# Optimization experiments

Hardware: AMD Instinct MI355X
Metric: run time of the kernel (lower is better)

Reference implementation:

```python
import jax, jax.numpy as jnp
import numpy as np


def setup_inputs() -> dict:
    key = jax.random.key(0)
    k1, k2, k3, k4 = jax.random.split(key, 4)
    n, c, p1, p2, r = 8, 3, 512, 512, 8
    X = jax.random.uniform(k1, (n, c, p1, p2), dtype=jnp.float32)
    S = jax.random.uniform(k2, (c, r), dtype=jnp.float32)
    S = S / (jnp.linalg.norm(S, axis=0, keepdims=True))  # unit-norm columns like S_init
    gamma = jax.random.uniform(k3, (1,), dtype=jnp.float32) * 1e-05
    lam = jax.random.uniform(k4, (1,), dtype=jnp.float32) * 1e-05
    return {"X": X, "S": S, "gamma": gamma, "lam": lam, "n_iter": 2}


def reference(X, S, gamma, lam, n_iter):
    n, c, p1, p2 = X.shape
    p = p1 * p2
    r = S.shape[1]
    Xf = X.reshape(n, c, p)
    gamma = jnp.abs(gamma)
    lam = jnp.abs(lam)
    Dt = jnp.zeros((n, r, p), dtype=X.dtype)
    x0 = jnp.mean(Xf, axis=2, keepdims=True)
    for _ in range(n_iter):
        # ---- D update (proximal gradient) ----
        SDt = jnp.einsum('cr,nrp->ncp', S, Dt)  # S @ Dt
        x0 = jnp.mean(Xf + SDt, axis=2, keepdims=True)  # [n,c,1]
        tau_D = 1.0 / jnp.sum(S * S)  # 1/||S||_F^2
        Dt = Dt - tau_D * jnp.einsum('cr,ncp->nrp', S, SDt + Xf - x0)
        S_nrm = jnp.linalg.norm(S, axis=0).reshape(1, r, 1)  # [1,r,1]
        Dt = jax.nn.relu(Dt - lam * gamma * tau_D * S_nrm)
        Dt_L2 = jnp.linalg.norm(Dt, axis=2, keepdims=True)  # [n,r,1]
        scl = jax.nn.relu(Dt_L2 - lam * tau_D * S_nrm)
        scl = scl / Dt_L2 + 1e-10  # faithful to source (eps added after divide)
        Dt = Dt * scl
        # ---- S update (proximal gradient) ----
        SDt = jnp.einsum('cr,nrp->ncp', S, Dt)
        x0 = jnp.mean(Xf + SDt, axis=2, keepdims=True)
        Dt_sum = jnp.sum(Dt, axis=2, keepdims=True)  # [n,r,1]
        tau_S = 1.0 / jnp.mean(jnp.sum(Dt * Dt, axis=(1, 2)))
        grad = jnp.mean(
            jnp.einsum('ncp,nqp->ncq', SDt + Xf, Dt)
            - x0 @ jnp.transpose(Dt_sum, (0, 2, 1)),
            axis=0)  # [c,r]
        S_grad = S - tau_S * grad
        Dt_nrm = jnp.mean(
            gamma * jnp.sum(jnp.abs(Dt), axis=2, keepdims=True)
            + jnp.linalg.norm(Dt, axis=2, keepdims=True), axis=0)  # [r,1]
        Sg_nrm = jnp.linalg.norm(S_grad, axis=0, keepdims=True)  # [1,r]
        scl_S = jax.nn.relu(Sg_nrm - lam * tau_S * Dt_nrm.T)
        scl_S = scl_S / (Sg_nrm + 1e-10)
        S = S_grad * scl_S
        # ---- unit-norm rescale (unit_norm_S=True) ----
        S_nrm2 = jnp.linalg.norm(S, axis=0, keepdims=True)  # [1,r]
        S = S / (S_nrm2 + 1e-10)
        Dt = Dt * (S_nrm2.reshape(1, r, 1) + 1e-10)
    return x0, S, Dt.reshape(n, r, p1, p2)
```

## Files before the change

kernel.cpp:

```cpp
#include <hip/hip_runtime.h>

constexpr int N = 8, C = 3, R = 8;
constexpr int P = 512 * 512;
constexpr int BLK = 256;
constexpr int NB = 128;
constexpr int PPB = P / NB;
constexpr int PITER = PPB / (BLK * 4);
constexpr int NBF = 256;
constexpr int PPBF = P / NBF;
constexpr int NK = 68;

typedef float f32x4 __attribute__((ext_vector_type(4)));

constexpr int W_XSUM  = 0;
constexpr int W_S1    = 32;
constexpr int W_F1    = 64;
constexpr int W_THR2  = 128;
constexpr int W_TAU2  = 136;
constexpr int W_SNRM2 = 144;
constexpr int W_X02   = 160;
constexpr int W_F2    = 192;
constexpr int W_RED   = 256;
constexpr int W_PART  = 1024;

#define XR8(M) M(0) M(1) M(2) M(3) M(4) M(5) M(6) M(7)
#define XTRI(M) \
  M(0,0) \
  M(1,0) M(1,1) \
  M(2,0) M(2,1) M(2,2) \
  M(3,0) M(3,1) M(3,2) M(3,3) \
  M(4,0) M(4,1) M(4,2) M(4,3) M(4,4) \
  M(5,0) M(5,1) M(5,2) M(5,3) M(5,4) M(5,5) \
  M(6,0) M(6,1) M(6,2) M(6,3) M(6,4) M(6,5) M(6,6) \
  M(7,0) M(7,1) M(7,2) M(7,3) M(7,4) M(7,5) M(7,6) M(7,7)
#define XCR(M) \
  M(0,0) M(0,1) M(0,2) M(0,3) M(0,4) M(0,5) M(0,6) M(0,7) \
  M(1,0) M(1,1) M(1,2) M(1,3) M(1,4) M(1,5) M(1,6) M(1,7) \
  M(2,0) M(2,1) M(2,2) M(2,3) M(2,4) M(2,5) M(2,6) M(2,7)

__device__ __forceinline__ float sld(float x) {
    return __uint_as_float(__builtin_amdgcn_readfirstlane(__float_as_uint(x)));
}
__device__ __forceinline__ float waveSum(float v) {
    #pragma unroll
    for (int o = 32; o > 0; o >>= 1) v += __shfl_down(v, o);
    return v;
}

__device__ __forceinline__ float rowSum16(float v) {
    int x;
    x = __builtin_amdgcn_update_dpp(0, __float_as_int(v), 0xB1, 0xF, 0xF, true);
    v += __int_as_float(x);
    x = __builtin_amdgcn_update_dpp(0, __float_as_int(v), 0x4E, 0xF, 0xF, true);
    v += __int_as_float(x);
    x = __builtin_amdgcn_update_dpp(0, __float_as_int(v), 0x124, 0xF, 0xF, true);
    v += __int_as_float(x);
    x = __builtin_amdgcn_update_dpp(0, __float_as_int(v), 0x128, 0xF, 0xF, true);
    v += __int_as_float(x);
    return v;
}

__global__ __launch_bounds__(BLK)
void k_xmean(const float* __restrict__ X, float* __restrict__ ws) {
    int nc = blockIdx.y;
    int t = threadIdx.x;
    size_t base = (size_t)nc * P + (size_t)blockIdx.x * 4096;
    float s = 0.f;
    #pragma unroll
    for (int i = 0; i < 4; ++i) {
        float4 q = *(const float4*)(X + base + (size_t)(i * BLK + t) * 4);
        s += (q.x + q.y) + (q.z + q.w);
    }
    __shared__ float red[16];
    s = rowSum16(s);
    if ((t & 15) == 0) red[t >> 4] = s;
    __syncthreads();
    if (t == 0) {
        float a = 0.f;
        #pragma unroll
        for (int g = 0; g < 16; ++g) a += red[g];
        atomicAdd(ws + W_XSUM + nc, a);
    }
}

__global__ __launch_bounds__(64)
void k_red(const float* __restrict__ part, float* __restrict__ ws) {
    int g = blockIdx.x, t = threadIdx.x;
    const float* p = part + (size_t)g * NB;
    float s = p[t] + p[t + 64];
    s = waveSum(s);
    if (t == 0) ws[W_RED + g] = s;
}

#define C_P1(r) const float p_##r = fmaxf(fmaf(-tau1c, fmaf(S0_0##r, tt0, fmaf(S0_1##r, tt1, S0_2##r * tt2)), -th1_##r), 0.f);
#define C_AL(r) const float a_##r = p_##r;
#define C_D2(r) const float d_##r = f1_##r * p_##r;
#define C_W(c)  const float w##c = fmaf(S1_##c##0, d_0, fmaf(S1_##c##1, d_1, fmaf(S1_##c##2, d_2, fmaf(S1_##c##3, d_3, fmaf(S1_##c##4, d_4, fmaf(S1_##c##5, d_5, fmaf(S1_##c##6, d_6, fmaf(S1_##c##7, d_7, tt##c + dx0_##c))))))));
#define C_A2(r) const float a_##r = fmaxf(fmaf(-tau2c, fmaf(S1_0##r, w0, fmaf(S1_1##r, w1, S1_2##r * w2)), d_##r - th2_##r), 0.f);
#define AC_T(q,r) tq_##q##_##r = fmaf(a_##r, a_##q, tq_##q##_##r);
#define AC_SM(r)  sm_##r += a_##r;
#define AC_V(c,q) vv_##c##_##q = fmaf(tt##c, a_##q, vv_##c##_##q);
#define GXc(q) (q).x
#define GYc(q) (q).y
#define GZc(q) (q).z
#define GWc(q) (q).w

template <int MODE>
__global__ __launch_bounds__(BLK)
void k_dstats(const float* __restrict__ X, const float* __restrict__ Sin,
              const float* __restrict__ gp, const float* __restrict__ lp,
              const float* __restrict__ ws, float* __restrict__ part) {
    const int n = blockIdx.y, t = threadIdx.x;
    const float lamv = fabsf(*lp), gamv = fabsf(*gp);
    const float invP = 1.0f / (float)P;

    float ssq0 = 0.f;
    #pragma unroll
    for (int i = 0; i < 24; ++i) { float v = Sin[i]; ssq0 = fmaf(v, v, ssq0); }
    const float tau1c = sld(1.0f / ssq0);
#define LD_TH1(r) const float th1_##r = sld(lamv * gamv * tau1c * sqrtf(fmaf(Sin[r], Sin[r], fmaf(Sin[8 + r], Sin[8 + r], Sin[16 + r] * Sin[16 + r]))));
    XR8(LD_TH1)
    const float x01_0 = sld(ws[W_XSUM + n * 3 + 0] * invP);
    const float x01_1 = sld(ws[W_XSUM + n * 3 + 1] * invP);
    const float x01_2 = sld(ws[W_XSUM + n * 3 + 2] * invP);
#define LD_S0(c,q) const float S0_##c##q = sld(Sin[(c) * 8 + (q)]);
    XCR(LD_S0)
#define LD_S1(c,q) const float S1_##c##q = (MODE >= 1) ? sld(ws[W_S1 + (c) * 8 + (q)]) : 0.f;
    XCR(LD_S1)
#define LD_F1(r)  const float f1_##r = (MODE >= 1) ? sld(ws[W_F1 + n * 8 + (r)]) : 0.f;
#define LD_TH2(r) const float th2_##r = (MODE >= 1) ? sld(ws[W_THR2 + (r)]) : 0.f;
    XR8(LD_F1) XR8(LD_TH2)
    const float tau2c = (MODE >= 1) ? sld(ws[W_TAU2]) : 0.f;
    const float dx0_0 = (MODE >= 1) ? sld(x01_0 - ws[W_X02 + n * 3 + 0]) : 0.f;
    const float dx0_1 = (MODE >= 1) ? sld(x01_1 - ws[W_X02 + n * 3 + 1]) : 0.f;
    const float dx0_2 = (MODE >= 1) ? sld(x01_2 - ws[W_X02 + n * 3 + 2]) : 0.f;

    const float* Xn = X + (size_t)n * C * P;
    const int rsel = t & 15, rowid = t >> 4;

#define SITE_T(GET) { \
    const float tt0 = GET(xv0) - x01_0; \
    const float tt1 = GET(xv1) - x01_1; \
    const float tt2 = GET(xv2) - x01_2; \
    XR8(C_P1) \
    if constexpr (MODE == 0) { XR8(C_AL) XTRI(AC_T) } \
    else { XR8(C_D2) C_W(0) C_W(1) C_W(2) XR8(C_A2) XTRI(AC_T) } }

#define SITE_SV(GET) { \
    const float tt0 = GET(xv0) - x01_0; \
    const float tt1 = GET(xv1) - x01_1; \
    const float tt2 = GET(xv2) - x01_2; \
    XR8(C_P1) \
    if constexpr (MODE == 0) { XR8(C_AL) XR8(AC_SM) XCR(AC_V) } \
    else { XR8(C_D2) C_W(0) C_W(1) C_W(2) XR8(C_A2) XR8(AC_SM) XCR(AC_V) } }

    if (blockIdx.z == 0) {
#define D_T(q,r) float tq_##q##_##r = 0.f;
        XTRI(D_T)
        #pragma unroll
        for (int it = 0; it < PITER; ++it) {
            size_t pbase = (size_t)blockIdx.x * PPB + (size_t)(it * BLK + t) * 4;
            float4 xv0 = *(const float4*)(Xn + 0 * (size_t)P + pbase);
            float4 xv1 = *(const float4*)(Xn + 1 * (size_t)P + pbase);
            float4 xv2 = *(const float4*)(Xn + 2 * (size_t)P + pbase);
            SITE_T(GXc) SITE_T(GYc) SITE_T(GZc) SITE_T(GWc)
        }
        __shared__ float redT[36][16];
#define RDT(q,r) { constexpr int kk = (q) * ((q) + 1) / 2 + (r); \
                   float v = rowSum16(tq_##q##_##r); \
                   if (rsel == (kk & 15)) redT[kk][rowid] = v; }
        XTRI(RDT)
        __syncthreads();
        if (t < 36) {
            const float* row = redT[t];
            float s = 0.f;
            #pragma unroll
            for (int g = 0; g < 16; ++g) s += row[g];
            part[((size_t)(8 + t) * N + n) * NB + blockIdx.x] = s;
        }
    } else {
#define D_SM(r)  float sm_##r = 0.f;
#define D_V(c,q) float vv_##c##_##q = 0.f;
        XR8(D_SM) XCR(D_V)
        #pragma unroll
        for (int it = 0; it < PITER; ++it) {
            size_t pbase = (size_t)blockIdx.x * PPB + (size_t)(it * BLK + t) * 4;
            float4 xv0 = *(const float4*)(Xn + 0 * (size_t)P + pbase);
            float4 xv1 = *(const float4*)(Xn + 1 * (size_t)P + pbase);
            float4 xv2 = *(const float4*)(Xn + 2 * (size_t)P + pbase);
            SITE_SV(GXc) SITE_SV(GYc) SITE_SV(GZc) SITE_SV(GWc)
        }
        __shared__ float redS[32][16];
#define RDS(r)   { constexpr int kk = (r); \
                   float v = rowSum16(sm_##r); \
                   if (rsel == (kk & 15)) redS[kk][rowid] = v; }
#define RDV(c,q) { constexpr int kk = 8 + (c) * 8 + (q); \
                   float v = rowSum16(vv_##c##_##q); \
                   if (rsel == (kk & 15)) redS[kk][rowid] = v; }
        XR8(RDS) XCR(RDV)
        __syncthreads();
        if (t < 32) {
            const float* row = redS[t];
            float s = 0.f;
            #pragma unroll
            for (int g = 0; g < 16; ++g) s += row[g];
            int krow = (t < 8) ? t : 44 + (t - 8);
            part[((size_t)krow * N + n) * NB + blockIdx.x] = s;
        }
    }
}

template <int IT>
__global__ __launch_bounds__(64)
void k_t23(const float* __restrict__ Sin, const float* __restrict__ gp,
           const float* __restrict__ lp, float* __restrict__ ws,
           float* __restrict__ x0_out, float* __restrict__ S_out) {
    const int t = threadIdx.x;
    const float invP = 1.0f / (float)P;
    const float lam_ = fabsf(*lp), gam_ = fabsf(*gp);
    __shared__ float sum_[N][R], T_[N][R][R], U_[N][C][R];
    __shared__ float scl_[N][R], L2_[N][R], x0s_[N][C], dtn_[R];
    __shared__ float Scur_[24], oS[24], oF[64], grad_[24], snrmI[8], pn_[8];
    __shared__ float tauS_, tauD_;
    for (int i = t; i < NK * N; i += 64) {
        int k = i / N, nn = i % N;
        float v = ws[W_RED + i];
        if (k < 8) sum_[nn][k] = v;
        else if (k < 44) {
            int m = k - 8; int q = 0;
            while ((q + 1) * (q + 2) / 2 <= m) ++q;
            int r = m - q * (q + 1) / 2;
            T_[nn][r][q] = v; T_[nn][q][r] = v;
        } else { int m = k - 44; U_[nn][m >> 3][m & 7] = v; }
    }
    if (t < 24) Scur_[t] = IT ? ws[W_S1 + t] : Sin[t];
    if (t == 0) {
        if (IT) tauD_ = ws[W_TAU2];
        else { float s = 0.f; for (int i = 0; i < 24; ++i) s += Sin[i] * Sin[i]; tauD_ = 1.0f / s; }
    }
    if (t < 8) {
        if (IT) snrmI[t] = ws[W_SNRM2 + t];
        else snrmI[t] = sqrtf(Sin[t] * Sin[t] + Sin[8 + t] * Sin[8 + t] + Sin[16 + t] * Sin[16 + t]);
    }
    __syncthreads();
    for (int i = t; i < N * C * R; i += 64) {
        int nn = i / 24, m = i % 24, c = m >> 3, q = m & 7;
        U_[nn][c][q] += ws[W_XSUM + nn * 3 + c] * invP * sum_[nn][q];
    }
    if (t < 64) {
        int nn = t >> 3, r = t & 7;
        float l2 = sqrtf(T_[nn][r][r]);
        float scl = fmaxf(l2 - lam_ * tauD_ * snrmI[r], 0.f) / l2 + 1e-10f;
        scl_[nn][r] = scl; L2_[nn][r] = l2;
    }
    __syncthreads();
    if (t == 0) {
        float tot = 0.f;
        for (int nn = 0; nn < N; ++nn)
            for (int r = 0; r < R; ++r)
                tot += scl_[nn][r] * scl_[nn][r] * T_[nn][r][r];
        tauS_ = (float)N / tot;
    }
    if (t < 24) {
        int nn = t / 3, c = t % 3;
        float acc = ws[W_XSUM + t] * invP;
        #pragma unroll
        for (int r = 0; r < R; ++r)
            acc += Scur_[c * R + r] * scl_[nn][r] * sum_[nn][r] * invP;
        x0s_[nn][c] = acc;
        if (IT == 1) x0_out[t] = acc;
    }
    if (t >= 32 && t < 40) {
        int r = t - 32;
        float a = 0.f;
        #pragma unroll
        for (int nn = 0; nn < N; ++nn)
            a += scl_[nn][r] * (gam_ * sum_[nn][r] + L2_[nn][r]);
        dtn_[r] = a * (1.0f / N);
    }
    __syncthreads();
    if (t < 24) {
        int c = t / 8, q = t % 8;
        float a = 0.f;
        #pragma unroll
        for (int nn = 0; nn < N; ++nn) {
            float m = U_[nn][c][q];
            #pragma unroll
            for (int r = 0; r < R; ++r)
                m += Scur_[c * R + r] * scl_[nn][r] * T_[nn][r][q];
            a += scl_[nn][q] * (m - x0s_[nn][c] * sum_[nn][q]);
        }
        grad_[t] = a * (1.0f / N);
    }
    __syncthreads();
    if (t == 0) {
        float Sg[24], Sn[24];
        #pragma unroll
        for (int i = 0; i < 24; ++i) Sg[i] = Scur_[i] - tauS_ * grad_[i];
        #pragma unroll
        for (int q = 0; q < 8; ++q) {
            float s2 = 0.f;
            #pragma unroll
            for (int c = 0; c < 3; ++c) s2 += Sg[c * 8 + q] * Sg[c * 8 + q];
            float sgn = sqrtf(s2);
            float s = fmaxf(sgn - lam_ * tauS_ * dtn_[q], 0.f) / (sgn + 1e-10f);
            #pragma unroll
            for (int c = 0; c < 3; ++c) Sn[c * 8 + q] = Sg[c * 8 + q] * s;
        }
        #pragma unroll
        for (int q = 0; q < 8; ++q) {
            float s2 = 0.f;
            #pragma unroll
            for (int c = 0; c < 3; ++c) s2 += Sn[c * 8 + q] * Sn[c * 8 + q];
            float n2 = sqrtf(s2);
            pn_[q] = n2;
            #pragma unroll
            for (int c = 0; c < 3; ++c) oS[c * 8 + q] = Sn[c * 8 + q] / (n2 + 1e-10f);
        }
        if (IT == 0) {
            float ssq = 0.f;
            #pragma unroll
            for (int i = 0; i < 24; ++i) ssq += oS[i] * oS[i];
            float tau2 = 1.0f / ssq;
            ws[W_TAU2] = tau2;
            #pragma unroll
            for (int r = 0; r < 8; ++r) {
                float cn = sqrtf(oS[r] * oS[r] + oS[8 + r] * oS[8 + r] + oS[16 + r] * oS[16 + r]);
                ws[W_SNRM2 + r] = cn;
                ws[W_THR2 + r] = lam_ * gam_ * tau2 * cn;
            }
        }
    }
    __syncthreads();
    if (t < 64) oF[t] = scl_[t >> 3][t & 7] * (pn_[t & 7] + 1e-10f);
    __syncthreads();
    if (IT == 0) {
        if (t < 24) {
            int nn = t / 3, c = t % 3;
            float acc = ws[W_XSUM + t] * invP;
            #pragma unroll
            for (int r = 0; r < R; ++r)
                acc += oS[c * R + r] * oF[nn * R + r] * sum_[nn][r] * invP;
            ws[W_X02 + t] = acc;
            ws[W_S1 + t] = oS[t];
        }
        if (t < 64) ws[W_F1 + t] = oF[t];
    } else {
        if (t < 24) S_out[t] = oS[t];
        if (t < 64) ws[W_F2 + t] = oF[t];
    }
}

__global__ __launch_bounds__(BLK)
void k_dfinal(const float* __restrict__ X, const float* __restrict__ Sin,
              const float* __restrict__ gp, const float* __restrict__ lp,
              const float* __restrict__ ws, float* __restrict__ Dt_out) {
    const int n = blockIdx.y, t = threadIdx.x;
    const float lamv = fabsf(*lp), gamv = fabsf(*gp);
    const float invP = 1.0f / (float)P;
    float ssq0 = 0.f;
    #pragma unroll
    for (int i = 0; i < 24; ++i) { float v = Sin[i]; ssq0 = fmaf(v, v, ssq0); }
    const float tau1c = sld(1.0f / ssq0);
    XR8(LD_TH1)
    const float x01_0 = sld(ws[W_XSUM + n * 3 + 0] * invP);
    const float x01_1 = sld(ws[W_XSUM + n * 3 + 1] * invP);
    const float x01_2 = sld(ws[W_XSUM + n * 3 + 2] * invP);
    XCR(LD_S0)
#define LD2_S1(c,q) const float S1_##c##q = sld(ws[W_S1 + (c) * 8 + (q)]);
#define LD2_F1(r)  const float f1_##r = sld(ws[W_F1 + n * 8 + (r)]);
#define LD2_TH2(r) const float th2_##r = sld(ws[W_THR2 + (r)]);
#define LD2_F2(r)  const float f2_##r = sld(ws[W_F2 + n * 8 + (r)]);
    XCR(LD2_S1) XR8(LD2_F1) XR8(LD2_TH2) XR8(LD2_F2)
    const float tau2c = sld(ws[W_TAU2]);
    const float dx0_0 = sld(x01_0 - ws[W_X02 + n * 3 + 0]);
    const float dx0_1 = sld(x01_1 - ws[W_X02 + n * 3 + 1]);
    const float dx0_2 = sld(x01_2 - ws[W_X02 + n * 3 + 2]);

    const float* Xn = X + (size_t)n * C * P;
    float* Dn = Dt_out + (size_t)n * R * P;

#define PXc(r) ov_##r.x = f2_##r * a_##r;
#define PYc(r) ov_##r.y = f2_##r * a_##r;
#define PZc(r) ov_##r.z = f2_##r * a_##r;
#define PWc(r) ov_##r.w = f2_##r * a_##r;
#define SITE_F(GET, PUTM) { \
    const float tt0 = GET(xv0) - x01_0; \
    const float tt1 = GET(xv1) - x01_1; \
    const float tt2 = GET(xv2) - x01_2; \
    XR8(C_P1) XR8(C_D2) C_W(0) C_W(1) C_W(2) XR8(C_A2) XR8(PUTM) }
#define D_OV(r) float4 ov_##r;
#define ST_O(r) *(float4*)(Dn + (size_t)(r) * P + pbase) = ov_##r;
    {
        size_t pbase = (size_t)blockIdx.x * PPBF + (size_t)t * 4;
        float4 xv0 = *(const float4*)(Xn + 0 * (size_t)P + pbase);
        float4 xv1 = *(const float4*)(Xn + 1 * (size_t)P + pbase);
        float4 xv2 = *(const float4*)(Xn + 2 * (size_t)P + pbase);
        XR8(D_OV)
        SITE_F(GXc, PXc) SITE_F(GYc, PYc) SITE_F(GZc, PZc) SITE_F(GWc, PWc)
        XR8(ST_O)
    }
}

extern "C" void kernel_launch(void* const* d_in, const int* in_sizes, int n_in,
                              void* d_out, int out_size, void* d_ws, size_t ws_size,
                              hipStream_t stream) {
    const float* X   = (const float*)d_in[0];
    const float* Sin = (const float*)d_in[1];
    const float* gam = (const float*)d_in[2];
    const float* lam = (const float*)d_in[3];
    float* out    = (float*)d_out;
    float* x0_out = out;
    float* S_out  = out + 24;
    float* Dt_out = out + 48;
    float* ws     = (float*)d_ws;
    float* part   = ws + W_PART;

    hipMemsetAsync(ws, 0, 24 * sizeof(float), stream);
    k_xmean<<<dim3(64, N * C), BLK, 0, stream>>>(X, ws);

    k_dstats<0><<<dim3(NB, N, 2), BLK, 0, stream>>>(X, Sin, gam, lam, ws, part);
    k_red<<<NK * N, 64, 0, stream>>>(part, ws);
    k_t23<0><<<1, 64, 0, stream>>>(Sin, gam, lam, ws, x0_out, S_out);

    k_dstats<1><<<dim3(NB, N, 2), BLK, 0, stream>>>(X, Sin, gam, lam, ws, part);
    k_red<<<NK * N, 64, 0, stream>>>(part, ws);
    k_t23<1><<<1, 64, 0, stream>>>(Sin, gam, lam, ws, x0_out, S_out);

    k_dfinal<<<dim3(NBF, N), BLK, 0, stream>>>(X, Sin, gam, lam, ws, Dt_out);
}
```

Baseline: 102.4 us.

## Replace partial-sum reduction kernels with atomics and recompute tiny solver per block

Per-block partial statistics are now accumulated directly with global atomicAdd instead of written to a partial buffer and reduced by a separate kernel. The single-block S-update kernels are removed, and their small math is recomputed redundantly at the start of every block of the next stats kernel and of the final kernel. This cuts the launch count from nine to five and removes two serialized tiny kernels. In exchange, every block repeats the tiny solver, including __syncthreads steps, before its main loop. Atomic accumulation also makes the floating-point summation order nondeterministic.

```diff
diff --git a/kernel.cpp b/kernel.cpp
--- a/kernel.cpp
+++ b/kernel.cpp
@@ -12,16 +12,10 @@
 
 typedef float f32x4 __attribute__((ext_vector_type(4)));
 
-constexpr int W_XSUM  = 0;
-constexpr int W_S1    = 32;
-constexpr int W_F1    = 64;
-constexpr int W_THR2  = 128;
-constexpr int W_TAU2  = 136;
-constexpr int W_SNRM2 = 144;
-constexpr int W_X02   = 160;
-constexpr int W_F2    = 192;
-constexpr int W_RED   = 256;
-constexpr int W_PART  = 1024;
+constexpr int W_XSUM = 0;
+constexpr int W_ACC1 = 32;
+constexpr int W_ACC2 = 608;
+constexpr int W_ZEND = 1152;
 
 #define XR8(M) M(0) M(1) M(2) M(3) M(4) M(5) M(6) M(7)
 #define XTRI(M) \
@@ -41,12 +35,6 @@
 __device__ __forceinline__ float sld(float x) {
     return __uint_as_float(__builtin_amdgcn_readfirstlane(__float_as_uint(x)));
 }
-__device__ __forceinline__ float waveSum(float v) {
-    #pragma unroll
-    for (int o = 32; o > 0; o >>= 1) v += __shfl_down(v, o);
-    return v;
-}
-
 __device__ __forceinline__ float rowSum16(float v) {
     int x;
     x = __builtin_amdgcn_update_dpp(0, __float_as_int(v), 0xB1, 0xF, 0xF, true);
@@ -83,13 +71,140 @@
     }
 }
 
-__global__ __launch_bounds__(64)
-void k_red(const float* __restrict__ part, float* __restrict__ ws) {
-    int g = blockIdx.x, t = threadIdx.x;
-    const float* p = part + (size_t)g * NB;
-    float s = p[t] + p[t + 64];
-    s = waveSum(s);
-    if (t == 0) ws[W_RED + g] = s;
+template <int IT>
+__device__ void t23_math(const float* __restrict__ accG, const float* __restrict__ SinG,
+                         const float* __restrict__ iS, const float* __restrict__ iTau,
+                         const float* __restrict__ iCN, const float* __restrict__ ws,
+                         float lam_, float gam_,
+                         float* oS, float* oF, float* oTH2, float* oTAU2,
+                         float* oCN, float* oX02, float* ox0s) {
+    const int t = threadIdx.x;
+    const float invP = 1.0f / (float)P;
+    __shared__ float sum_[N][R], T_[N][R][R], U_[N][C][R];
+    __shared__ float scl_[N][R], L2_[N][R], x0s_[N][C], dtn_[R];
+    __shared__ float Scur_[24], grad_[24], snrmI[8], pn_[8];
+    __shared__ float tauS_, tauD_;
+    for (int i = t; i < NK * N; i += BLK) {
+        int k = i / N, nn = i % N;
+        float v = accG[i];
+        if (k < 8) sum_[nn][k] = v;
+        else if (k < 44) {
+            int m = k - 8; int q = 0;
+            while ((q + 1) * (q + 2) / 2 <= m) ++q;
+            int r = m - q * (q + 1) / 2;
+            T_[nn][r][q] = v; T_[nn][q][r] = v;
+        } else { int m = k - 44; U_[nn][m >> 3][m & 7] = v; }
+    }
+    if (t < 24) Scur_[t] = IT ? iS[t] : SinG[t];
+    if (t == 0) {
+        if (IT) tauD_ = iTau[0];
+        else { float s = 0.f; for (int i = 0; i < 24; ++i) s += SinG[i] * SinG[i]; tauD_ = 1.0f / s; }
+    }
+    if (t < 8) {
+        if (IT) snrmI[t] = iCN[t];
+        else snrmI[t] = sqrtf(SinG[t] * SinG[t] + SinG[8 + t] * SinG[8 + t] + SinG[16 + t] * SinG[16 + t]);
+    }
+    __syncthreads();
+    for (int i = t; i < N * C * R; i += BLK) {
+        int nn = i / 24, m = i % 24, c = m >> 3, q = m & 7;
+        U_[nn][c][q] += ws[W_XSUM + nn * 3 + c] * invP * sum_[nn][q];
+    }
+    if (t < 64) {
+        int nn = t >> 3, r = t & 7;
+        float l2 = sqrtf(T_[nn][r][r]);
+        float scl = fmaxf(l2 - lam_ * tauD_ * snrmI[r], 0.f) / l2 + 1e-10f;
+        scl_[nn][r] = scl; L2_[nn][r] = l2;
+    }
+    __syncthreads();
+    if (t == 0) {
+        float tot = 0.f;
+        for (int nn = 0; nn < N; ++nn)
+            for (int r = 0; r < R; ++r)
+                tot += scl_[nn][r] * scl_[nn][r] * T_[nn][r][r];
+        tauS_ = (float)N / tot;
+    }
+    if (t < 24) {
+        int nn = t / 3, c = t % 3;
+        float acc = ws[W_XSUM + t] * invP;
+        #pragma unroll
+        for (int r = 0; r < R; ++r)
+            acc += Scur_[c * R + r] * scl_[nn][r] * sum_[nn][r] * invP;
+        x0s_[nn][c] = acc;
+        if (IT == 1) ox0s[t] = acc;
+    }
+    if (t >= 32 && t < 40) {
+        int r = t - 32;
+        float a = 0.f;
+        #pragma unroll
+        for (int nn = 0; nn < N; ++nn)
+            a += scl_[nn][r] * (gam_ * sum_[nn][r] + L2_[nn][r]);
+        dtn_[r] = a * (1.0f / N);
+    }
+    __syncthreads();
+    if (t < 24) {
+        int c = t / 8, q = t % 8;
+        float a = 0.f;
+        #pragma unroll
+        for (int nn = 0; nn < N; ++nn) {
+            float m = U_[nn][c][q];
+            #pragma unroll
+            for (int r = 0; r < R; ++r)
+                m += Scur_[c * R + r] * scl_[nn][r] * T_[nn][r][q];
+            a += scl_[nn][q] * (m - x0s_[nn][c] * sum_[nn][q]);
+        }
+        grad_[t] = a * (1.0f / N);
+    }
+    __syncthreads();
+    if (t == 0) {
+        float Sg[24], Sn[24];
+        #pragma unroll
+        for (int i = 0; i < 24; ++i) Sg[i] = Scur_[i] - tauS_ * grad_[i];
+        #pragma unroll
+        for (int q = 0; q < 8; ++q) {
+            float s2 = 0.f;
+            #pragma unroll
+            for (int c = 0; c < 3; ++c) s2 += Sg[c * 8 + q] * Sg[c * 8 + q];
+            float sgn = sqrtf(s2);
+            float s = fmaxf(sgn - lam_ * tauS_ * dtn_[q], 0.f) / (sgn + 1e-10f);
+            #pragma unroll
+            for (int c = 0; c < 3; ++c) Sn[c * 8 + q] = Sg[c * 8 + q] * s;
+        }
+        #pragma unroll
+        for (int q = 0; q < 8; ++q) {
+            float s2 = 0.f;
+            #pragma unroll
+            for (int c = 0; c < 3; ++c) s2 += Sn[c * 8 + q] * Sn[c * 8 + q];
+            float n2 = sqrtf(s2);
+            pn_[q] = n2;
+            #pragma unroll
+            for (int c = 0; c < 3; ++c) oS[c * 8 + q] = Sn[c * 8 + q] / (n2 + 1e-10f);
+        }
+        if (IT == 0) {
+            float ssq = 0.f;
+            #pragma unroll
+            for (int i = 0; i < 24; ++i) ssq += oS[i] * oS[i];
+            float tau2 = 1.0f / ssq;
+            oTAU2[0] = tau2;
+            #pragma unroll
+            for (int r = 0; r < 8; ++r) {
+                float cn = sqrtf(oS[r] * oS[r] + oS[8 + r] * oS[8 + r] + oS[16 + r] * oS[16 + r]);
+                oCN[r] = cn;
+                oTH2[r] = lam_ * gam_ * tau2 * cn;
+            }
+        }
+    }
+    __syncthreads();
+    if (t < 64) oF[t] = scl_[t >> 3][t & 7] * (pn_[t & 7] + 1e-10f);
+    __syncthreads();
+    if (IT == 0 && t < 24) {
+        int nn = t / 3, c = t % 3;
+        float acc = ws[W_XSUM + t] * invP;
+        #pragma unroll
+        for (int r = 0; r < R; ++r)
+            acc += oS[c * R + r] * oF[nn * R + r] * sum_[nn][r] * invP;
+        oX02[t] = acc;
+    }
+    __syncthreads();
 }
 
 #define C_P1(r) const float p_##r = fmaxf(fmaf(-tau1c, fmaf(S0_0##r, tt0, fmaf(S0_1##r, tt1, S0_2##r * tt2)), -th1_##r), 0.f);
@@ -109,10 +224,16 @@
 __global__ __launch_bounds__(BLK)
 void k_dstats(const float* __restrict__ X, const float* __restrict__ Sin,
               const float* __restrict__ gp, const float* __restrict__ lp,
-              const float* __restrict__ ws, float* __restrict__ part) {
+              float* __restrict__ ws) {
     const int n = blockIdx.y, t = threadIdx.x;
     const float lamv = fabsf(*lp), gamv = fabsf(*gp);
     const float invP = 1.0f / (float)P;
+
+    __shared__ float oS[24], oF[64], oTH2[8], oTAU2[1], oCN[8], oX02[24];
+    if constexpr (MODE == 1) {
+        t23_math<0>(ws + W_ACC1, Sin, nullptr, nullptr, nullptr, ws, lamv, gamv,
+                    oS, oF, oTH2, oTAU2, oCN, oX02, nullptr);
+    }
 
     float ssq0 = 0.f;
     #pragma unroll
@@ -125,18 +246,19 @@
     const float x01_2 = sld(ws[W_XSUM + n * 3 + 2] * invP);
 #define LD_S0(c,q) const float S0_##c##q = sld(Sin[(c) * 8 + (q)]);
     XCR(LD_S0)
-#define LD_S1(c,q) const float S1_##c##q = (MODE >= 1) ? sld(ws[W_S1 + (c) * 8 + (q)]) : 0.f;
+#define LD_S1(c,q) const float S1_##c##q = (MODE >= 1) ? sld(oS[(c) * 8 + (q)]) : 0.f;
     XCR(LD_S1)
-#define LD_F1(r)  const float f1_##r = (MODE >= 1) ? sld(ws[W_F1 + n * 8 + (r)]) : 0.f;
-#define LD_TH2(r) const float th2_##r = (MODE >= 1) ? sld(ws[W_THR2 + (r)]) : 0.f;
+#define LD_F1(r)  const float f1_##r = (MODE >= 1) ? sld(oF[n * 8 + (r)]) : 0.f;
+#define LD_TH2(r) const float th2_##r = (MODE >= 1) ? sld(oTH2[(r)]) : 0.f;
     XR8(LD_F1) XR8(LD_TH2)
-    const float tau2c = (MODE >= 1) ? sld(ws[W_TAU2]) : 0.f;
-    const float dx0_0 = (MODE >= 1) ? sld(x01_0 - ws[W_X02 + n * 3 + 0]) : 0.f;
-    const float dx0_1 = (MODE >= 1) ? sld(x01_1 - ws[W_X02 + n * 3 + 1]) : 0.f;
-    const float dx0_2 = (MODE >= 1) ? sld(x01_2 - ws[W_X02 + n * 3 + 2]) : 0.f;
+    const float tau2c = (MODE >= 1) ? sld(oTAU2[0]) : 0.f;
+    const float dx0_0 = (MODE >= 1) ? sld(x01_0 - oX02[n * 3 + 0]) : 0.f;
+    const float dx0_1 = (MODE >= 1) ? sld(x01_1 - oX02[n * 3 + 1]) : 0.f;
+    const float dx0_2 = (MODE >= 1) ? sld(x01_2 - oX02[n * 3 + 2]) : 0.f;
 
     const float* Xn = X + (size_t)n * C * P;
     const int rsel = t & 15, rowid = t >> 4;
+    float* accOut = ws + (MODE == 0 ? W_ACC1 : W_ACC2);
 
 #define SITE_T(GET) { \
     const float tt0 = GET(xv0) - x01_0; \
@@ -176,7 +298,7 @@
             float s = 0.f;
             #pragma unroll
             for (int g = 0; g < 16; ++g) s += row[g];
-            part[((size_t)(8 + t) * N + n) * NB + blockIdx.x] = s;
+            atomicAdd(accOut + (8 + t) * N + n, s);
         }
     } else {
 #define D_SM(r)  float sm_##r = 0.f;
@@ -205,159 +327,28 @@
             #pragma unroll
             for (int g = 0; g < 16; ++g) s += row[g];
             int krow = (t < 8) ? t : 44 + (t - 8);
-            part[((size_t)krow * N + n) * NB + blockIdx.x] = s;
-        }
-    }
-}
-
-template <int IT>
-__global__ __launch_bounds__(64)
-void k_t23(const float* __restrict__ Sin, const float* __restrict__ gp,
-           const float* __restrict__ lp, float* __restrict__ ws,
-           float* __restrict__ x0_out, float* __restrict__ S_out) {
-    const int t = threadIdx.x;
-    const float invP = 1.0f / (float)P;
-    const float lam_ = fabsf(*lp), gam_ = fabsf(*gp);
-    __shared__ float sum_[N][R], T_[N][R][R], U_[N][C][R];
-    __shared__ float scl_[N][R], L2_[N][R], x0s_[N][C], dtn_[R];
-    __shared__ float Scur_[24], oS[24], oF[64], grad_[24], snrmI[8], pn_[8];
-    __shared__ float tauS_, tauD_;
-    for (int i = t; i < NK * N; i += 64) {
-        int k = i / N, nn = i % N;
-        float v = ws[W_RED + i];
-        if (k < 8) sum_[nn][k] = v;
-        else if (k < 44) {
-            int m = k - 8; int q = 0;
-            while ((q + 1) * (q + 2) / 2 <= m) ++q;
-            int r = m - q * (q + 1) / 2;
-            T_[nn][r][q] = v; T_[nn][q][r] = v;
-        } else { int m = k - 44; U_[nn][m >> 3][m & 7] = v; }
-    }
-    if (t < 24) Scur_[t] = IT ? ws[W_S1 + t] : Sin[t];
-    if (t == 0) {
-        if (IT) tauD_ = ws[W_TAU2];
-        else { float s = 0.f; for (int i = 0; i < 24; ++i) s += Sin[i] * Sin[i]; tauD_ = 1.0f / s; }
-    }
-    if (t < 8) {
-        if (IT) snrmI[t] = ws[W_SNRM2 + t];
-        else snrmI[t] = sqrtf(Sin[t] * Sin[t] + Sin[8 + t] * Sin[8 + t] + Sin[16 + t] * Sin[16 + t]);
-    }
-    __syncthreads();
-    for (int i = t; i < N * C * R; i += 64) {
-        int nn = i / 24, m = i % 24, c = m >> 3, q = m & 7;
-        U_[nn][c][q] += ws[W_XSUM + nn * 3 + c] * invP * sum_[nn][q];
-    }
-    if (t < 64) {
-        int nn = t >> 3, r = t & 7;
-        float l2 = sqrtf(T_[nn][r][r]);
-        float scl = fmaxf(l2 - lam_ * tauD_ * snrmI[r], 0.f) / l2 + 1e-10f;
-        scl_[nn][r] = scl; L2_[nn][r] = l2;
-    }
-    __syncthreads();
-    if (t == 0) {
-        float tot = 0.f;
-        for (int nn = 0; nn < N; ++nn)
-            for (int r = 0; r < R; ++r)
-                tot += scl_[nn][r] * scl_[nn][r] * T_[nn][r][r];
-        tauS_ = (float)N / tot;
-    }
-    if (t < 24) {
-        int nn = t / 3, c = t % 3;
-        float acc = ws[W_XSUM + t] * invP;
-        #pragma unroll
-        for (int r = 0; r < R; ++r)
-            acc += Scur_[c * R + r] * scl_[nn][r] * sum_[nn][r] * invP;
-        x0s_[nn][c] = acc;
-        if (IT == 1) x0_out[t] = acc;
-    }
-    if (t >= 32 && t < 40) {
-        int r = t - 32;
-        float a = 0.f;
-        #pragma unroll
-        for (int nn = 0; nn < N; ++nn)
-            a += scl_[nn][r] * (gam_ * sum_[nn][r] + L2_[nn][r]);
-        dtn_[r] = a * (1.0f / N);
-    }
-    __syncthreads();
-    if (t < 24) {
-        int c = t / 8, q = t % 8;
-        float a = 0.f;
-        #pragma unroll
-        for (int nn = 0; nn < N; ++nn) {
-            float m = U_[nn][c][q];
-            #pragma unroll
-            for (int r = 0; r < R; ++r)
-                m += Scur_[c * R + r] * scl_[nn][r] * T_[nn][r][q];
-            a += scl_[nn][q] * (m - x0s_[nn][c] * sum_[nn][q]);
-        }
-        grad_[t] = a * (1.0f / N);
-    }
-    __syncthreads();
-    if (t == 0) {
-        float Sg[24], Sn[24];
-        #pragma unroll
-        for (int i = 0; i < 24; ++i) Sg[i] = Scur_[i] - tauS_ * grad_[i];
-        #pragma unroll
-        for (int q = 0; q < 8; ++q) {
-            float s2 = 0.f;
-            #pragma unroll
-            for (int c = 0; c < 3; ++c) s2 += Sg[c * 8 + q] * Sg[c * 8 + q];
-            float sgn = sqrtf(s2);
-            float s = fmaxf(sgn - lam_ * tauS_ * dtn_[q], 0.f) / (sgn + 1e-10f);
-            #pragma unroll
-            for (int c = 0; c < 3; ++c) Sn[c * 8 + q] = Sg[c * 8 + q] * s;
-        }
-        #pragma unroll
-        for (int q = 0; q < 8; ++q) {
-            float s2 = 0.f;
-            #pragma unroll
-            for (int c = 0; c < 3; ++c) s2 += Sn[c * 8 + q] * Sn[c * 8 + q];
-            float n2 = sqrtf(s2);
-            pn_[q] = n2;
-            #pragma unroll
-            for (int c = 0; c < 3; ++c) oS[c * 8 + q] = Sn[c * 8 + q] / (n2 + 1e-10f);
-        }
-        if (IT == 0) {
-            float ssq = 0.f;
-            #pragma unroll
-            for (int i = 0; i < 24; ++i) ssq += oS[i] * oS[i];
-            float tau2 = 1.0f / ssq;
-            ws[W_TAU2] = tau2;
-            #pragma unroll
-            for (int r = 0; r < 8; ++r) {
-                float cn = sqrtf(oS[r] * oS[r] + oS[8 + r] * oS[8 + r] + oS[16 + r] * oS[16 + r]);
-                ws[W_SNRM2 + r] = cn;
-                ws[W_THR2 + r] = lam_ * gam_ * tau2 * cn;
-            }
-        }
-    }
-    __syncthreads();
-    if (t < 64) oF[t] = scl_[t >> 3][t & 7] * (pn_[t & 7] + 1e-10f);
-    __syncthreads();
-    if (IT == 0) {
-        if (t < 24) {
-            int nn = t / 3, c = t % 3;
-            float acc = ws[W_XSUM + t] * invP;
-            #pragma unroll
-            for (int r = 0; r < R; ++r)
-                acc += oS[c * R + r] * oF[nn * R + r] * sum_[nn][r] * invP;
-            ws[W_X02 + t] = acc;
-            ws[W_S1 + t] = oS[t];
-        }
-        if (t < 64) ws[W_F1 + t] = oF[t];
-    } else {
-        if (t < 24) S_out[t] = oS[t];
-        if (t < 64) ws[W_F2 + t] = oF[t];
+            atomicAdd(accOut + krow * N + n, s);
+        }
     }
 }
 
 __global__ __launch_bounds__(BLK)
 void k_dfinal(const float* __restrict__ X, const float* __restrict__ Sin,
               const float* __restrict__ gp, const float* __restrict__ lp,
-              const float* __restrict__ ws, float* __restrict__ Dt_out) {
+              float* __restrict__ ws, float* __restrict__ Dt_out,
+              float* __restrict__ x0_out, float* __restrict__ S_out) {
     const int n = blockIdx.y, t = threadIdx.x;
     const float lamv = fabsf(*lp), gamv = fabsf(*gp);
     const float invP = 1.0f / (float)P;
+
+    __shared__ float oS[24], oF[64], oTH2[8], oTAU2[1], oCN[8], oX02[24];
+    __shared__ float oS2[24], oF2[64], oTH2b[8], oTAU2b[1], oCNb[8], oX02b[24], ox0s[24];
+    t23_math<0>(ws + W_ACC1, Sin, nullptr, nullptr, nullptr, ws, lamv, gamv,
+                oS, oF, oTH2, oTAU2, oCN, oX02, nullptr);
+    t23_math<1>(ws + W_ACC2, nullptr, oS, oTAU2, oCN, ws, lamv, gamv,
+                oS2, oF2, oTH2b, oTAU2b, oCNb, oX02b, ox0s);
+    if (blockIdx.x == 0 && n == 0 && t < 24) { x0_out[t] = ox0s[t]; S_out[t] = oS2[t]; }
+
     float ssq0 = 0.f;
     #pragma unroll
     for (int i = 0; i < 24; ++i) { float v = Sin[i]; ssq0 = fmaf(v, v, ssq0); }
@@ -367,15 +358,15 @@
     const float x01_1 = sld(ws[W_XSUM + n * 3 + 1] * invP);
     const float x01_2 = sld(ws[W_XSUM + n * 3 + 2] * invP);
     XCR(LD_S0)
-#define LD2_S1(c,q) const float S1_##c##q = sld(ws[W_S1 + (c) * 8 + (q)]);
-#define LD2_F1(r)  const float f1_##r = sld(ws[W_F1 + n * 8 + (r)]);
-#define LD2_TH2(r) const float th2_##r = sld(ws[W_THR2 + (r)]);
-#define LD2_F2(r)  const float f2_##r = sld(ws[W_F2 + n * 8 + (r)]);
-    XCR(LD2_S1) XR8(LD2_F1) XR8(LD2_TH2) XR8(LD2_F2)
-    const float tau2c = sld(ws[W_TAU2]);
-    const float dx0_0 = sld(x01_0 - ws[W_X02 + n * 3 + 0]);
-    const float dx0_1 = sld(x01_1 - ws[W_X02 + n * 3 + 1]);
-    const float dx0_2 = sld(x01_2 - ws[W_X02 + n * 3 + 2]);
+#define LDF_S1(c,q) const float S1_##c##q = sld(oS[(c) * 8 + (q)]);
+#define LDF_F1(r)  const float f1_##r = sld(oF[n * 8 + (r)]);
+#define LDF_TH2(r) const float th2_##r = sld(oTH2[(r)]);
+#define LDF_F2(r)  const float f2_##r = sld(oF2[n * 8 + (r)]);
+    XCR(LDF_S1) XR8(LDF_F1) XR8(LDF_TH2) XR8(LDF_F2)
+    const float tau2c = sld(oTAU2[0]);
+    const float dx0_0 = sld(x01_0 - oX02[n * 3 + 0]);
+    const float dx0_1 = sld(x01_1 - oX02[n * 3 + 1]);
+    const float dx0_2 = sld(x01_2 - oX02[n * 3 + 2]);
 
     const float* Xn = X + (size_t)n * C * P;
     float* Dn = Dt_out + (size_t)n * R * P;
@@ -414,18 +405,10 @@
     float* S_out  = out + 24;
     float* Dt_out = out + 48;
     float* ws     = (float*)d_ws;
-    float* part   = ws + W_PART;
-
-    hipMemsetAsync(ws, 0, 24 * sizeof(float), stream);
+
+    hipMemsetAsync(ws, 0, W_ZEND * sizeof(float), stream);
     k_xmean<<<dim3(64, N * C), BLK, 0, stream>>>(X, ws);
-
-    k_dstats<0><<<dim3(NB, N, 2), BLK, 0, stream>>>(X, Sin, gam, lam, ws, part);
-    k_red<<<NK * N, 64, 0, stream>>>(part, ws);
-    k_t23<0><<<1, 64, 0, stream>>>(Sin, gam, lam, ws, x0_out, S_out);
-
-    k_dstats<1><<<dim3(NB, N, 2), BLK, 0, stream>>>(X, Sin, gam, lam, ws, part);
-    k_red<<<NK * N, 64, 0, stream>>>(part, ws);
-    k_t23<1><<<1, 64, 0, stream>>>(Sin, gam, lam, ws, x0_out, S_out);
-
-    k_dfinal<<<dim3(NBF, N), BLK, 0, stream>>>(X, Sin, gam, lam, ws, Dt_out);
-}
+    k_dstats<0><<<dim3(NB, N, 2), BLK, 0, stream>>>(X, Sin, gam, lam, ws);
+    k_dstats<1><<<dim3(NB, N, 2), BLK, 0, stream>>>(X, Sin, gam, lam, ws);
+    k_dfinal<<<dim3(NBF, N), BLK, 0, stream>>>(X, Sin, gam, lam, ws, Dt_out, x0_out, S_out);
+}
```

Result: slower. 175.8 us (+71.6%).
